# Optimization experiments

Hardware: AMD Instinct MI355X
Metric: run time of the kernel (lower is better)

The kernel has to match this reference:

```python
import jax, jax.numpy as jnp
import numpy as np

N_NODES = 50000
N_EDGES = 800000
N_GRAPHS = 256
IN_DIM = 64
HID = 128


def setup_inputs() -> dict:
    key = jax.random.key(0)
    ks = jax.random.split(key, 16)
    x = jax.random.normal(ks[0], (N_NODES, IN_DIM), dtype=jnp.float32)
    edge_index = jax.random.randint(ks[1], (2, N_EDGES), 0, N_NODES)
    batch = jnp.sort(jax.random.randint(ks[2], (N_NODES,), 0, N_GRAPHS))
    edge_attr = jax.random.uniform(ks[3], (N_EDGES,), dtype=jnp.float32)

    def lin(k, out_d, in_d):
        s = 1.0 / np.sqrt(in_d)
        return jax.random.uniform(k, (out_d, in_d), minval=-s, maxval=s, dtype=jnp.float32)

    params = {
        'W1r': lin(ks[4], HID, IN_DIM), 'b1': jnp.zeros((HID,), jnp.float32), 'W1root': lin(ks[5], HID, IN_DIM),
        'W2r': lin(ks[6], HID, HID), 'b2': jnp.zeros((HID,), jnp.float32), 'W2root': lin(ks[7], HID, HID),
        'W3r': lin(ks[8], HID // 2, HID), 'b3': jnp.zeros((HID // 2,), jnp.float32), 'W3root': lin(ks[9], HID // 2, HID),
        'Wm1': lin(ks[10], HID // 4, HID // 2), 'bm1': jnp.zeros((HID // 4,), jnp.float32),
        'Wm2': lin(ks[11], HID // 8, HID // 4), 'bm2': jnp.zeros((HID // 8,), jnp.float32),
        'Wm3': lin(ks[12], 1, HID // 8), 'bm3': jnp.zeros((1,), jnp.float32),
    }
    return dict(x=x, edge_index=edge_index, batch=batch, edge_attr=edge_attr, **params)


def _graph_conv(x, src, dst, ew, Wr, br, Wroot):
    # PyG GraphConv(aggr='add'): lin_rel(scatter_add(x[src]*w)) + lin_root(x)
    msg = x[src] * ew[:, None]                      # [E, d] gather + scale
    agg = jax.ops.segment_sum(msg, dst, num_segments=x.shape[0])  # [N, d]
    return agg @ Wr.T + br + x @ Wroot.T


def reference(x, edge_index, batch, edge_attr,
              W1r, b1, W1root, W2r, b2, W2root, W3r, b3, W3root,
              Wm1, bm1, Wm2, bm2, Wm3, bm3):
    src, dst = edge_index[0], edge_index[1]
    # eval mode: dropouts are identity
    h = jnp.tanh(_graph_conv(x, src, dst, edge_attr, W1r, b1, W1root))
    h = jnp.tanh(_graph_conv(h, src, dst, edge_attr, W2r, b2, W2root))
    h = jnp.tanh(_graph_conv(h, src, dst, edge_attr, W3r, b3, W3root))
    # global add pool over graphs
    g = jax.ops.segment_sum(h, batch, num_segments=N_GRAPHS)      # [G, hid//2]
    g = jax.nn.relu(g @ Wm1.T + bm1)
    g = jax.nn.relu(g @ Wm2.T + bm2)
    return g @ Wm3.T + bm3                                        # [G, 1]
```

## Files before the change

kernel.cpp:

```cpp
#include <hip/hip_runtime.h>

#define N_NODES 50000
#define N_EDGES 800000
#define N_GRAPHS 256
#define SCAN_B ((N_NODES + 255) / 256)
#define FILL_GROUPS 8
#define NPG (N_NODES / FILL_GROUPS)

typedef __attribute__((ext_vector_type(8))) short bf16x8;
typedef __attribute__((ext_vector_type(4))) float f32x4;

__device__ inline unsigned short f2bf(float f) {
    unsigned int u = __float_as_uint(f);
    u += 0x7fff + ((u >> 16) & 1);
    return (unsigned short)(u >> 16);
}
__device__ inline float bf2f(unsigned short h) {
    return __uint_as_float(((unsigned int)h) << 16);
}
__device__ inline float fast_tanh(float x) {
    return 1.0f - 2.0f / (__expf(2.0f * x) + 1.0f);
}

__global__ void pack_w_kernel(const float* __restrict__ s0, const float* __restrict__ s1,
                              int K0, int KTOT, int nconcat,
                              unsigned short* __restrict__ hi, unsigned short* __restrict__ lo)
{
    const int idx = blockIdx.x * 256 + threadIdx.x;
    if (idx >= 128 * KTOT) return;
    const int c = idx / KTOT, k = idx % KTOT;
    float v;
    if (nconcat) v = (c < 64) ? s0[c * KTOT + k] : s1[(c - 64) * KTOT + k];
    else         v = (k < K0) ? s0[c * K0 + k]   : s1[c * K0 + (k - K0)];
    const unsigned short h = f2bf(v);
    hi[idx] = h;
    lo[idx] = f2bf(v - bf2f(h));
}

__global__ void cvt_bf16_kernel(const float* __restrict__ in,
                                unsigned short* __restrict__ out, int n4)
{
    const int i = blockIdx.x * 256 + threadIdx.x;
    if (i >= n4) return;
    const float4 v = ((const float4*)in)[i];
    ((ushort4*)out)[i] = make_ushort4(f2bf(v.x), f2bf(v.y), f2bf(v.z), f2bf(v.w));
}

template<int KF32, int KB16, bool OUTSPLIT, bool ACT>
__global__ __launch_bounds__(256)
void gemm_mfma(const float* __restrict__ Af, int fstr,
               const unsigned short* __restrict__ Ab, int bstr,
               const unsigned short* __restrict__ Bhi, const unsigned short* __restrict__ Blo,
               const float* __restrict__ bias,
               unsigned short* __restrict__ C16, float* __restrict__ Cf)
{
    constexpr int KTOT = KF32 + KB16;
    constexpr int NCHF = KF32 / 32;
    constexpr int NCH  = KTOT / 32;

    __shared__ __align__(16) unsigned short lah[64 * 40];
    __shared__ __align__(16) unsigned short lal[64 * 40];
    __shared__ __align__(16) unsigned short lbh[128 * 40];
    __shared__ __align__(16) unsigned short lbl[128 * 40];

    const int tid = threadIdx.x;
    const int w = tid >> 6;
    const int lane = tid & 63;
    const int lrow = lane & 15;
    const int lkb = lane >> 4;
    const int m0 = blockIdx.x * 64;

    f32x4 acc[4][2] = {};

    for (int ch = 0; ch < NCH; ++ch) {
        const bool isF = (ch < NCHF);
        const int bk0 = ch * 32;

        __syncthreads();
        if (isF) {
            const int ak0 = ch * 32;
#pragma unroll
            for (int p = 0; p < 2; ++p) {
                const int f = tid + p * 256;
                const int r = f >> 3;
                const int q = f & 7;
                int row = m0 + r; if (row >= N_NODES) row = N_NODES - 1;
                const float4 v = *(const float4*)&Af[(long)row * fstr + ak0 + q * 4];
                const unsigned short h0 = f2bf(v.x), h1 = f2bf(v.y), h2 = f2bf(v.z), h3 = f2bf(v.w);
                *(ushort4*)&lah[r * 40 + q * 4] = make_ushort4(h0, h1, h2, h3);
                *(ushort4*)&lal[r * 40 + q * 4] =
                    make_ushort4(f2bf(v.x - bf2f(h0)), f2bf(v.y - bf2f(h1)),
                                 f2bf(v.z - bf2f(h2)), f2bf(v.w - bf2f(h3)));
            }
        } else {
            const int ak0 = (ch - NCHF) * 32;
            const int r = tid >> 2;
            const int q = tid & 3;
            int row = m0 + r; if (row >= N_NODES) row = N_NODES - 1;
            *(uint4*)&lah[r * 40 + q * 8] = *(const uint4*)&Ab[(long)row * bstr + ak0 + q * 8];
        }
#pragma unroll
        for (int p = 0; p < 2; ++p) {
            const int f = tid + p * 256;
            const int r = f >> 2;
            const int q = f & 3;
            const long g = (long)r * KTOT + bk0 + q * 8;
            *(uint4*)&lbh[r * 40 + q * 8] = *(const uint4*)&Bhi[g];
            *(uint4*)&lbl[r * 40 + q * 8] = *(const uint4*)&Blo[g];
        }
        __syncthreads();

        const int bo0 = (w * 32 + lrow) * 40 + lkb * 8;
        const int bo1 = bo0 + 16 * 40;
        const bf16x8 bh0 = *(const bf16x8*)&lbh[bo0];
        const bf16x8 bh1 = *(const bf16x8*)&lbh[bo1];
        const bf16x8 bl0 = *(const bf16x8*)&lbl[bo0];
        const bf16x8 bl1 = *(const bf16x8*)&lbl[bo1];
#pragma unroll
        for (int m = 0; m < 4; ++m) {
            const int ao = (m * 16 + lrow) * 40 + lkb * 8;
            const bf16x8 ah = *(const bf16x8*)&lah[ao];
            acc[m][0] = __builtin_amdgcn_mfma_f32_16x16x32_bf16(ah, bh0, acc[m][0], 0, 0, 0);
            acc[m][1] = __builtin_amdgcn_mfma_f32_16x16x32_bf16(ah, bh1, acc[m][1], 0, 0, 0);
            acc[m][0] = __builtin_amdgcn_mfma_f32_16x16x32_bf16(ah, bl0, acc[m][0], 0, 0, 0);
            acc[m][1] = __builtin_amdgcn_mfma_f32_16x16x32_bf16(ah, bl1, acc[m][1], 0, 0, 0);
            if (isF) {
                const bf16x8 al = *(const bf16x8*)&lal[ao];
                acc[m][0] = __builtin_amdgcn_mfma_f32_16x16x32_bf16(al, bh0, acc[m][0], 0, 0, 0);
                acc[m][1] = __builtin_amdgcn_mfma_f32_16x16x32_bf16(al, bh1, acc[m][1], 0, 0, 0);
            }
        }
    }

    const int c0 = w * 32 + lrow;
    if (!OUTSPLIT) {
        const float bb0 = bias[c0], bb1 = bias[c0 + 16];
#pragma unroll
        for (int m = 0; m < 4; ++m) {
#pragma unroll
            for (int r = 0; r < 4; ++r) {
                const int row = m0 + m * 16 + lkb * 4 + r;
                if (row < N_NODES) {
                    float v0 = acc[m][0][r] + bb0;
                    float v1 = acc[m][1][r] + bb1;
                    if (ACT) { v0 = fast_tanh(v0); v1 = fast_tanh(v1); }
                    C16[(long)row * 128 + c0]      = f2bf(v0);
                    C16[(long)row * 128 + c0 + 16] = f2bf(v1);
                }
            }
        }
    } else if (c0 < 64) {
#pragma unroll
        for (int m = 0; m < 4; ++m) {
#pragma unroll
            for (int r = 0; r < 4; ++r) {
                const int row = m0 + m * 16 + lkb * 4 + r;
                if (row < N_NODES) {
                    C16[(long)row * 64 + c0]      = f2bf(acc[m][0][r]);
                    C16[(long)row * 64 + c0 + 16] = f2bf(acc[m][1][r]);
                }
            }
        }
    } else {
        const float bb0 = bias[c0 - 64], bb1 = bias[c0 - 48];
#pragma unroll
        for (int m = 0; m < 4; ++m) {
#pragma unroll
            for (int r = 0; r < 4; ++r) {
                const int row = m0 + m * 16 + lkb * 4 + r;
                if (row < N_NODES) {
                    Cf[(long)row * 64 + c0 - 64] = acc[m][0][r] + bb0;
                    Cf[(long)row * 64 + c0 - 48] = acc[m][1][r] + bb1;
                }
            }
        }
    }
}

__global__ void count_kernel(const int* __restrict__ ei, int* __restrict__ count)
{
    const int e = blockIdx.x * blockDim.x + threadIdx.x;
    if (e < N_EDGES) atomicAdd(&count[ei[N_EDGES + e]], 1);
}

__global__ __launch_bounds__(256)
void scan_blocks_kernel(const int* __restrict__ count, int* __restrict__ blocksum)
{
    __shared__ int red[256];
    const int i = blockIdx.x * 256 + threadIdx.x;
    red[threadIdx.x] = (i < N_NODES) ? count[i] : 0;
    __syncthreads();
#pragma unroll
    for (int d = 128; d > 0; d >>= 1) {
        if (threadIdx.x < d) red[threadIdx.x] += red[threadIdx.x + d];
        __syncthreads();
    }
    if (threadIdx.x == 0) blocksum[blockIdx.x] = red[0];
}

__global__ __launch_bounds__(256)
void scan_base_kernel(const int* __restrict__ blocksum, int* __restrict__ blockbase)
{
    __shared__ int s[256];
    const int t = threadIdx.x;
    const int own = (t < SCAN_B) ? blocksum[t] : 0;
    s[t] = own;
    __syncthreads();
#pragma unroll
    for (int d = 1; d < 256; d <<= 1) {
        const int v = (t >= d) ? s[t - d] : 0;
        __syncthreads();
        s[t] += v;
        __syncthreads();
    }
    if (t < SCAN_B) blockbase[t] = s[t] - own;
}

__global__ __launch_bounds__(256)
void scan_final_kernel(const int* __restrict__ count, const int* __restrict__ blockbase,
                       int* __restrict__ offsets, int* __restrict__ cursor)
{
    __shared__ int s[256];
    const int t = threadIdx.x;
    const int i = blockIdx.x * 256 + t;
    const int v = (i < N_NODES) ? count[i] : 0;
    s[t] = v;
    __syncthreads();
#pragma unroll
    for (int d = 1; d < 256; d <<= 1) {
        const int u = (t >= d) ? s[t - d] : 0;
        __syncthreads();
        s[t] += u;
        __syncthreads();
    }
    if (i < N_NODES) {
        const int off = blockbase[blockIdx.x] + s[t] - v;
        offsets[i] = off;
        cursor[i] = off;
    }
    if (i == 0) offsets[N_NODES] = N_EDGES;
}

__global__ __launch_bounds__(256)
void fill_kernel(const int* __restrict__ ei, const float* __restrict__ ew,
                 int* __restrict__ cursor, uint2* __restrict__ rec)
{
    const int g = blockIdx.x & (FILL_GROUPS - 1);
    const int q = blockIdx.x >> 3;
    const int nlo = g * NPG;
    const int nhi = nlo + NPG;
    const int stride = (gridDim.x >> 3) * 256;
    for (int e = q * 256 + threadIdx.x; e < N_EDGES; e += stride) {
        const int t = ei[N_EDGES + e];
        if (t >= nlo && t < nhi) {
            const int pos = atomicAdd(&cursor[t], 1);
            rec[pos] = make_uint2((unsigned)ei[e], __float_as_uint(ew[e]));
        }
    }
}

template<int D>
__global__ __launch_bounds__(256)
void gather_agg(const unsigned short* __restrict__ feat, int stride,
                const int* __restrict__ offsets, const uint2* __restrict__ rec,
                float* __restrict__ agg)
{
    constexpr int LPN = D / 8;
    constexpr int NPB = 256 / LPN;
    const int lane = threadIdx.x % LPN;
    const int slot = threadIdx.x / LPN;
    const int n = blockIdx.x * NPB + slot;
    if (n >= N_NODES) return;
    const int lo = offsets[n], hi = offsets[n + 1];
    const int j = lane * 8;
    float a0[8] = {}, a1[8] = {};
    int e = lo;
    for (; e + 1 < hi; e += 2) {
        const uint2 r0 = rec[e];
        const uint2 r1 = rec[e + 1];
        const bf16x8 v0 = *(const bf16x8*)&feat[(long)r0.x * stride + j];
        const bf16x8 v1 = *(const bf16x8*)&feat[(long)r1.x * stride + j];
        const float w0 = __uint_as_float(r0.y);
        const float w1 = __uint_as_float(r1.y);
#pragma unroll
        for (int k = 0; k < 8; ++k) {
            a0[k] = fmaf(bf2f((unsigned short)v0[k]), w0, a0[k]);
            a1[k] = fmaf(bf2f((unsigned short)v1[k]), w1, a1[k]);
        }
    }
    if (e < hi) {
        const uint2 r = rec[e];
        const bf16x8 v = *(const bf16x8*)&feat[(long)r.x * stride + j];
        const float w = __uint_as_float(r.y);
#pragma unroll
        for (int k = 0; k < 8; ++k)
            a0[k] = fmaf(bf2f((unsigned short)v[k]), w, a0[k]);
    }
    *(float4*)&agg[(long)n * D + j] =
        make_float4(a0[0] + a1[0], a0[1] + a1[1], a0[2] + a1[2], a0[3] + a1[3]);
    *(float4*)&agg[(long)n * D + j + 4] =
        make_float4(a0[4] + a1[4], a0[5] + a1[5], a0[6] + a1[6], a0[7] + a1[7]);
}

__global__ void gstart_kernel(const int* __restrict__ batch, int* __restrict__ gstart)
{
    const int g = threadIdx.x;
    int lo = 0, hi = N_NODES;
    while (lo < hi) { const int mid = (lo + hi) >> 1; if (batch[mid] < g) lo = mid + 1; else hi = mid; }
    gstart[g] = lo;
    if (g == 0) gstart[N_GRAPHS] = N_NODES;
}

__global__ __launch_bounds__(256)
void pool_seg_kernel(const float* __restrict__ agg3, const float* __restrict__ root3,
                     const int* __restrict__ gstart, float* __restrict__ g)
{
    const int gi = blockIdx.x;
    const int c = threadIdx.x & 63;
    const int sub = threadIdx.x >> 6;
    const int lo = gstart[gi], hi = gstart[gi + 1];
    float acc = 0.f;
    for (int n = lo + sub; n < hi; n += 4)
        acc += fast_tanh(agg3[(long)n * 64 + c] + root3[(long)n * 64 + c]);
    __shared__ float red[256];
    red[threadIdx.x] = acc;
    __syncthreads();
    if (sub == 0) g[gi * 64 + c] = red[c] + red[64 + c] + red[128 + c] + red[192 + c];
}

__global__ __launch_bounds__(64)
void mlp_kernel(const float* __restrict__ g,
                const float* __restrict__ Wm1, const float* __restrict__ bm1,
                const float* __restrict__ Wm2, const float* __restrict__ bm2,
                const float* __restrict__ Wm3, const float* __restrict__ bm3,
                float* __restrict__ out)
{
    const int gi = blockIdx.x;
    const int l = threadIdx.x;
    __shared__ float gr[64], h1[32], h2[16];
    gr[l] = g[gi * 64 + l];
    __syncthreads();
    if (l < 32) {
        float a = bm1[l];
        const float* w = Wm1 + l * 64;
        for (int k = 0; k < 64; ++k) a = fmaf(gr[k], w[k], a);
        h1[l] = fmaxf(a, 0.f);
    }
    __syncthreads();
    if (l < 16) {
        float a = bm2[l];
        const float* w = Wm2 + l * 32;
        for (int k = 0; k < 32; ++k) a = fmaf(h1[k], w[k], a);
        h2[l] = fmaxf(a, 0.f);
    }
    __syncthreads();
    if (l == 0) {
        float a = bm3[0];
        for (int k = 0; k < 16; ++k) a = fmaf(h2[k], Wm3[k], a);
        out[gi] = a;
    }
}

extern "C" void kernel_launch(void* const* d_in, const int* in_sizes, int n_in,
                              void* d_out, int out_size, void* d_ws, size_t ws_size,
                              hipStream_t stream) {
    const float* x      = (const float*)d_in[0];
    const int*   ei     = (const int*)  d_in[1];
    const int*   batch  = (const int*)  d_in[2];
    const float* ew     = (const float*)d_in[3];
    const float* W1r    = (const float*)d_in[4];
    const float* b1     = (const float*)d_in[5];
    const float* W1root = (const float*)d_in[6];
    const float* W2r    = (const float*)d_in[7];
    const float* b2     = (const float*)d_in[8];
    const float* W2root = (const float*)d_in[9];
    const float* W3r    = (const float*)d_in[10];
    const float* b3     = (const float*)d_in[11];
    const float* W3root = (const float*)d_in[12];
    const float* Wm1    = (const float*)d_in[13];
    const float* bm1    = (const float*)d_in[14];
    const float* Wm2    = (const float*)d_in[15];
    const float* bm2    = (const float*)d_in[16];
    const float* Wm3    = (const float*)d_in[17];
    const float* bm3    = (const float*)d_in[18];
    float* out = (float*)d_out;

    float* agg1  = (float*)d_ws;
    float* agg2  = agg1 + (long)N_NODES * 64;
    float* POOL  = agg2 + (long)N_NODES * 128;
    int*   count    = (int*)(POOL + N_GRAPHS * 64);
    int*   offsets  = count + N_NODES;
    int*   cursor   = offsets + N_NODES + 1;
    int*   gstart   = cursor + N_NODES + 1;
    int*   blocksum = gstart + N_GRAPHS + 1;
    int*   blockbase= blocksum + SCAN_B;
    uintptr_t wp = ((uintptr_t)(blockbase + SCAN_B) + 15) & ~(uintptr_t)15;
    uint2* rec = (uint2*)wp;
    unsigned short* xb  = (unsigned short*)(rec + N_EDGES);
    unsigned short* h1b = xb + (long)N_NODES * 64;
    unsigned short* h2b = h1b + (long)N_NODES * 128;
    unsigned short* Bh1 = h2b + (long)N_NODES * 128;
    unsigned short* Bl1 = Bh1 + 128 * 128;
    unsigned short* Bh2 = Bl1 + 128 * 128;
    unsigned short* Bl2 = Bh2 + 128 * 256;
    unsigned short* Bh3 = Bl2 + 128 * 256;
    unsigned short* Bl3 = Bh3 + 128 * 128;
    unsigned short* y3b = (unsigned short*)agg2;
    float* root3 = agg2 + (long)N_NODES * 64;
    float* agg3  = agg1;

    const int gemm_grid = (N_NODES + 63) / 64;
    const int egrid = (N_EDGES + 255) / 256;

    pack_w_kernel<<<(128 * 128 + 255) / 256, 256, 0, stream>>>(W1r, W1root, 64, 128, 0, Bh1, Bl1);
    pack_w_kernel<<<(128 * 256 + 255) / 256, 256, 0, stream>>>(W2r, W2root, 128, 256, 0, Bh2, Bl2);
    pack_w_kernel<<<(128 * 128 + 255) / 256, 256, 0, stream>>>(W3r, W3root, 128, 128, 1, Bh3, Bl3);
    cvt_bf16_kernel<<<(N_NODES * 64 / 4 + 255) / 256, 256, 0, stream>>>(x, xb, N_NODES * 64 / 4);

    hipMemsetAsync(count, 0, N_NODES * sizeof(int), stream);
    count_kernel<<<egrid, 256, 0, stream>>>(ei, count);
    scan_blocks_kernel<<<SCAN_B, 256, 0, stream>>>(count, blocksum);
    scan_base_kernel<<<1, 256, 0, stream>>>(blocksum, blockbase);
    scan_final_kernel<<<SCAN_B, 256, 0, stream>>>(count, blockbase, offsets, cursor);
    fill_kernel<<<2048, 256, 0, stream>>>(ei, ew, cursor, rec);
    gstart_kernel<<<1, 256, 0, stream>>>(batch, gstart);

    gather_agg<64><<<(N_NODES + 31) / 32, 256, 0, stream>>>(xb, 64, offsets, rec, agg1);
    gemm_mfma<64, 64, false, true><<<gemm_grid, 256, 0, stream>>>(
        agg1, 64, xb, 64, Bh1, Bl1, b1, h1b, nullptr);

    gather_agg<128><<<(N_NODES + 15) / 16, 256, 0, stream>>>(h1b, 128, offsets, rec, agg2);
    gemm_mfma<128, 128, false, true><<<gemm_grid, 256, 0, stream>>>(
        agg2, 128, h1b, 128, Bh2, Bl2, b2, h2b, nullptr);

    gemm_mfma<0, 128, true, false><<<gemm_grid, 256, 0, stream>>>(
        nullptr, 0, h2b, 128, Bh3, Bl3, b3, y3b, root3);
    gather_agg<64><<<(N_NODES + 31) / 32, 256, 0, stream>>>(y3b, 64, offsets, rec, agg3);

    pool_seg_kernel<<<N_GRAPHS, 256, 0, stream>>>(agg3, root3, gstart, POOL);
    mlp_kernel<<<N_GRAPHS, 64, 0, stream>>>(POOL, Wm1, bm1, Wm2, bm2, Wm3, bm3, out);
}
```

Measured before the change: 268.7 us.

## Split neighbor aggregation into 32-column passes to shrink gather working set

```diff
diff --git a/kernel.cpp b/kernel.cpp
--- a/kernel.cpp
+++ b/kernel.cpp
@@ -259,20 +259,17 @@
     }
 }
 
-template<int D>
-__global__ __launch_bounds__(256)
-void gather_agg(const unsigned short* __restrict__ feat, int stride,
-                const int* __restrict__ offsets, const uint2* __restrict__ rec,
-                float* __restrict__ agg)
-{
-    constexpr int LPN = D / 8;
-    constexpr int NPB = 256 / LPN;
-    const int lane = threadIdx.x % LPN;
-    const int slot = threadIdx.x / LPN;
-    const int n = blockIdx.x * NPB + slot;
+__global__ __launch_bounds__(256)
+void gather_pass(const unsigned short* __restrict__ feat, int stride, int colbase,
+                 const int* __restrict__ offsets, const uint2* __restrict__ rec,
+                 float* __restrict__ agg, int dstr)
+{
+    const int lane = threadIdx.x & 3;
+    const int slot = threadIdx.x >> 2;
+    const int n = blockIdx.x * 64 + slot;
     if (n >= N_NODES) return;
     const int lo = offsets[n], hi = offsets[n + 1];
-    const int j = lane * 8;
+    const int j = colbase + lane * 8;
     float a0[8] = {}, a1[8] = {};
     int e = lo;
     for (; e + 1 < hi; e += 2) {
@@ -296,9 +293,9 @@
         for (int k = 0; k < 8; ++k)
             a0[k] = fmaf(bf2f((unsigned short)v[k]), w, a0[k]);
     }
-    *(float4*)&agg[(long)n * D + j] =
+    *(float4*)&agg[(long)n * dstr + j] =
         make_float4(a0[0] + a1[0], a0[1] + a1[1], a0[2] + a1[2], a0[3] + a1[3]);
-    *(float4*)&agg[(long)n * D + j + 4] =
+    *(float4*)&agg[(long)n * dstr + j + 4] =
         make_float4(a0[4] + a1[4], a0[5] + a1[5], a0[6] + a1[6], a0[7] + a1[7]);
 }
 
@@ -410,6 +407,7 @@
     float* agg3  = agg1;
 
     const int gemm_grid = (N_NODES + 63) / 64;
+    const int gat_grid  = (N_NODES + 63) / 64;
     const int egrid = (N_EDGES + 255) / 256;
 
     pack_w_kernel<<<(128 * 128 + 255) / 256, 256, 0, stream>>>(W1r, W1root, 64, 128, 0, Bh1, Bl1);
@@ -425,17 +423,22 @@
     fill_kernel<<<2048, 256, 0, stream>>>(ei, ew, cursor, rec);
     gstart_kernel<<<1, 256, 0, stream>>>(batch, gstart);
 
-    gather_agg<64><<<(N_NODES + 31) / 32, 256, 0, stream>>>(xb, 64, offsets, rec, agg1);
+    gather_pass<<<gat_grid, 256, 0, stream>>>(xb, 64, 0,  offsets, rec, agg1, 64);
+    gather_pass<<<gat_grid, 256, 0, stream>>>(xb, 64, 32, offsets, rec, agg1, 64);
     gemm_mfma<64, 64, false, true><<<gemm_grid, 256, 0, stream>>>(
         agg1, 64, xb, 64, Bh1, Bl1, b1, h1b, nullptr);
 
-    gather_agg<128><<<(N_NODES + 15) / 16, 256, 0, stream>>>(h1b, 128, offsets, rec, agg2);
+    gather_pass<<<gat_grid, 256, 0, stream>>>(h1b, 128, 0,  offsets, rec, agg2, 128);
+    gather_pass<<<gat_grid, 256, 0, stream>>>(h1b, 128, 32, offsets, rec, agg2, 128);
+    gather_pass<<<gat_grid, 256, 0, stream>>>(h1b, 128, 64, offsets, rec, agg2, 128);
+    gather_pass<<<gat_grid, 256, 0, stream>>>(h1b, 128, 96, offsets, rec, agg2, 128);
     gemm_mfma<128, 128, false, true><<<gemm_grid, 256, 0, stream>>>(
         agg2, 128, h1b, 128, Bh2, Bl2, b2, h2b, nullptr);
 
     gemm_mfma<0, 128, true, false><<<gemm_grid, 256, 0, stream>>>(
         nullptr, 0, h2b, 128, Bh3, Bl3, b3, y3b, root3);
-    gather_agg<64><<<(N_NODES + 31) / 32, 256, 0, stream>>>(y3b, 64, offsets, rec, agg3);
+    gather_pass<<<gat_grid, 256, 0, stream>>>(y3b, 64, 0,  offsets, rec, agg3, 64);
+    gather_pass<<<gat_grid, 256, 0, stream>>>(y3b, 64, 32, offsets, rec, agg3, 64);
 
     pool_seg_kernel<<<N_GRAPHS, 256, 0, stream>>>(agg3, root3, gstart, POOL);
     mlp_kernel<<<N_GRAPHS, 64, 0, stream>>>(POOL, Wm1, bm1, Wm2, bm2, Wm3, bm3, out);
```

New measurement: 346.6 us. 1.29x slower.
